# Kernel tuning notes

Measured on AMD Instinct MI355X. Metric: run time of the kernel, lower is better.

## Reference

```python
import jax, jax.numpy as jnp
import numpy as np

OMEGA = 1.5

def _sine(x, W, b, omega=OMEGA):
    return jnp.sin(omega * (x @ W.T + b))

def setup_inputs() -> dict:
    key = jax.random.key(0)
    ks = jax.random.split(key, 17)
    I = J = K = 384
    mid, R = 256, 100
    s = 0.05  # small init scale, mimics uniform(-1/in, 1/in) style init
    return {
        "A_input": jax.random.normal(ks[0], (I, 1), jnp.float32),
        "B_input": jax.random.normal(ks[1], (J, 1), jnp.float32),
        "C_input": jax.random.normal(ks[2], (K, 1), jnp.float32),
        "A_W1": jax.random.normal(ks[3], (mid, 1), jnp.float32) * s,
        "A_b1": jax.random.normal(ks[4], (mid,), jnp.float32) * s,
        "A_W2": jax.random.normal(ks[5], (R, mid), jnp.float32) * s,
        "A_b2": jax.random.normal(ks[6], (R,), jnp.float32) * s,
        "B_W1": jax.random.normal(ks[7], (mid, 1), jnp.float32) * s,
        "B_b1": jax.random.normal(ks[8], (mid,), jnp.float32) * s,
        "B_W2": jax.random.normal(ks[9], (R, mid), jnp.float32) * s,
        "B_b2": jax.random.normal(ks[10], (R,), jnp.float32) * s,
        "C_W1": jax.random.normal(ks[11], (mid, 1), jnp.float32) * s,
        "C_b1": jax.random.normal(ks[12], (mid,), jnp.float32) * s,
        "C_W2": jax.random.normal(ks[13], (mid, mid), jnp.float32) * s,
        "C_b2": jax.random.normal(ks[14], (mid,), jnp.float32) * s,
        "C_W3": jax.random.normal(ks[15], (R, mid), jnp.float32) * s,
        "C_b3": jax.random.normal(ks[16], (R,), jnp.float32) * s,
    }

def reference(A_input, B_input, C_input,
              A_W1, A_b1, A_W2, A_b2,
              B_W1, B_b1, B_W2, B_b2,
              C_W1, C_b1, C_W2, C_b2, C_W3, C_b3):
    # Factor networks
    A = _sine(A_input, A_W1, A_b1) @ A_W2.T + A_b2                  # [I, R]
    B = _sine(B_input, B_W1, B_b1) @ B_W2.T + B_b2                  # [J, R]
    C = _sine(_sine(C_input, C_W1, C_b1), C_W2, C_b2) @ C_W3.T + C_b3  # [K, R]
    # The frozen core is super-diagonal (core[r,r,r]=1), so the permute/matmul
    # chain reduces exactly to the CP contraction sum_r A[i,r]*B[j,r]*C[k,r].
    return jnp.einsum('ir,jr,kr->ijk', A, B, C)  # [I, J, K]
```

## Files before the change

kernel.cpp:

```cpp
#include <hip/hip_runtime.h>
#include <hip/hip_bf16.h>

#define RR 100
#define MID 256
#define NN 384
#define KP 128

typedef __attribute__((ext_vector_type(8))) __bf16 bf16x8;
typedef __attribute__((ext_vector_type(4))) float floatx4;
typedef unsigned short ushort_t;

#define SW(row, ch) ((((row) << 7)) + ((((ch) ^ ((row) & 15))) << 3))

__device__ __forceinline__ ushort_t f2bf(float f) {
  __hip_bfloat16 h = __float2bfloat16(f);
  return __builtin_bit_cast(ushort_t, h);
}

__global__ __launch_bounds__(256) void factors_kernel(
    const float* __restrict__ xA, const float* __restrict__ xB,
    const float* __restrict__ xC,
    const float* __restrict__ AW1, const float* __restrict__ Ab1,
    const float* __restrict__ AW2, const float* __restrict__ Ab2,
    const float* __restrict__ BW1, const float* __restrict__ Bb1,
    const float* __restrict__ BW2, const float* __restrict__ Bb2,
    const float* __restrict__ CW1, const float* __restrict__ Cb1,
    const float* __restrict__ CW2, const float* __restrict__ Cb2,
    const float* __restrict__ CW3, const float* __restrict__ Cb3,
    float* __restrict__ Af, float* __restrict__ Bf,
    ushort_t* __restrict__ Cbf) {
  __shared__ float h[MID];
  __shared__ float h2[MID];
  const int i = blockIdx.x;
  const int net = blockIdx.y;
  const int t = threadIdx.x;

  const float* x  = (net == 0) ? xA  : (net == 1) ? xB  : xC;
  const float* W1 = (net == 0) ? AW1 : (net == 1) ? BW1 : CW1;
  const float* b1 = (net == 0) ? Ab1 : (net == 1) ? Bb1 : Cb1;

  const float xv = x[i];
  h[t] = sinf(1.5f * (xv * W1[t] + b1[t]));
  __syncthreads();

  const float* hlast = h;
  if (net == 2) {
    float acc = Cb2[t];
    const float* __restrict__ w = &CW2[t * MID];
#pragma unroll 4
    for (int m = 0; m < MID; m += 4) {
      const float4 wv = *(const float4*)&w[m];
      const float4 hv = *(const float4*)&h[m];
      acc += hv.x * wv.x;
      acc += hv.y * wv.y;
      acc += hv.z * wv.z;
      acc += hv.w * wv.w;
    }
    h2[t] = sinf(1.5f * acc);
    __syncthreads();
    hlast = h2;
  }

  const float* W2 = (net == 0) ? AW2 : (net == 1) ? BW2 : CW3;
  const float* b2 = (net == 0) ? Ab2 : (net == 1) ? Bb2 : Cb3;

  if (t < KP) {
    float v = 0.0f;
    if (t < RR) {
      float acc = b2[t];
      const float* __restrict__ w = &W2[t * MID];
#pragma unroll 4
      for (int m = 0; m < MID; m += 4) {
        const float4 wv = *(const float4*)&w[m];
        const float4 hv = *(const float4*)&hlast[m];
        acc += hv.x * wv.x;
        acc += hv.y * wv.y;
        acc += hv.z * wv.z;
        acc += hv.w * wv.w;
      }
      v = acc;
    }
    if (net == 0)      Af[i * KP + t] = v;
    else if (net == 1) Bf[i * KP + t] = v;
    else               Cbf[i * KP + t] = f2bf(v);
  }
}

__global__ __launch_bounds__(256, 3) void cp_mfma(
    const float* __restrict__ Af, const float* __restrict__ Bf,
    const ushort_t* __restrict__ Cbf, float* __restrict__ out) {
  __shared__ ushort_t Wt[64 * KP];
  __shared__ ushort_t Ct[128 * KP];

  const int bid = blockIdx.x;
  const int swz = (bid & 7) * 288 + (bid >> 3);
  const int i   = swz / 6;
  const int j0  = (swz % 6) * 64;
  const int t   = threadIdx.x;

  {
    const int jx = t >> 2;
    const int q  = t & 3;
    const float* __restrict__ arow = Af + (size_t)i * KP + q * 32;
    const float* __restrict__ brow = Bf + (size_t)(j0 + jx) * KP + q * 32;
#pragma unroll
    for (int c = 0; c < 4; ++c) {
      const float4 a0 = *(const float4*)(arow + c * 8);
      const float4 a1 = *(const float4*)(arow + c * 8 + 4);
      const float4 b0 = *(const float4*)(brow + c * 8);
      const float4 b1 = *(const float4*)(brow + c * 8 + 4);
      uint4 wv;
      wv.x = (unsigned)f2bf(a0.x * b0.x) | ((unsigned)f2bf(a0.y * b0.y) << 16);
      wv.y = (unsigned)f2bf(a0.z * b0.z) | ((unsigned)f2bf(a0.w * b0.w) << 16);
      wv.z = (unsigned)f2bf(a1.x * b1.x) | ((unsigned)f2bf(a1.y * b1.y) << 16);
      wv.w = (unsigned)f2bf(a1.z * b1.z) | ((unsigned)f2bf(a1.w * b1.w) << 16);
      *(uint4*)&Wt[SW(jx, q * 4 + c)] = wv;
    }
  }

  const int lane = t & 63;
  const int w    = t >> 6;
  const int m16  = lane & 15;
  const int g    = lane >> 4;
  const int jrow = j0 + w * 16 + m16;
  const size_t obase = (size_t)i * NN * NN + (size_t)jrow * NN;

#pragma unroll 1
  for (int kt = 0; kt < 3; ++kt) {
    __syncthreads();

#pragma unroll
    for (int it = 0; it < 8; ++it) {
      const int idx = t + 256 * it;
      const int row = idx >> 4;
      const int ch  = idx & 15;
      *(uint4*)&Ct[SW(row, ch)] =
          *(const uint4*)&Cbf[(size_t)(kt * 128 + row) * KP + ch * 8];
    }
    __syncthreads();

    floatx4 acc[8];
#pragma unroll
    for (int kf = 0; kf < 8; ++kf) acc[kf] = (floatx4)0.0f;

#pragma unroll
    for (int ks = 0; ks < 4; ++ks) {
      const bf16x8 wfr = *(const bf16x8*)&Wt[SW(w * 16 + m16, ks * 4 + g)];
#pragma unroll
      for (int kf = 0; kf < 8; ++kf) {
        const bf16x8 cf = *(const bf16x8*)&Ct[SW(kf * 16 + m16, ks * 4 + g)];
        acc[kf] = __builtin_amdgcn_mfma_f32_16x16x32_bf16(
            cf, wfr, acc[kf], 0, 0, 0);
      }
    }

    const int kb = kt * 128 + g * 4;
#pragma unroll
    for (int kf = 0; kf < 8; ++kf) {
      *(floatx4*)&out[obase + kb + kf * 16] = acc[kf];
    }
  }
}

extern "C" void kernel_launch(void* const* d_in, const int* in_sizes, int n_in,
                              void* d_out, int out_size, void* d_ws, size_t ws_size,
                              hipStream_t stream) {
  const float* A_input = (const float*)d_in[0];
  const float* B_input = (const float*)d_in[1];
  const float* C_input = (const float*)d_in[2];
  const float* A_W1 = (const float*)d_in[3];
  const float* A_b1 = (const float*)d_in[4];
  const float* A_W2 = (const float*)d_in[5];
  const float* A_b2 = (const float*)d_in[6];
  const float* B_W1 = (const float*)d_in[7];
  const float* B_b1 = (const float*)d_in[8];
  const float* B_W2 = (const float*)d_in[9];
  const float* B_b2 = (const float*)d_in[10];
  const float* C_W1 = (const float*)d_in[11];
  const float* C_b1 = (const float*)d_in[12];
  const float* C_W2 = (const float*)d_in[13];
  const float* C_b2 = (const float*)d_in[14];
  const float* C_W3 = (const float*)d_in[15];
  const float* C_b3 = (const float*)d_in[16];

  float* Af = (float*)d_ws;
  float* Bf = Af + NN * KP;
  ushort_t* Cbf = (ushort_t*)(Bf + NN * KP);

  dim3 fgrid(NN, 3);
  factors_kernel<<<fgrid, 256, 0, stream>>>(
      A_input, B_input, C_input,
      A_W1, A_b1, A_W2, A_b2,
      B_W1, B_b1, B_W2, B_b2,
      C_W1, C_b1, C_W2, C_b2, C_W3, C_b3,
      Af, Bf, Cbf);

  cp_mfma<<<dim3((NN / 64) * NN), 256, 0, stream>>>(Af, Bf, Cbf, (float*)d_out);
}
```

Baseline: 292.8 us.

## Register-prefetch next C tile while computing current tile in cp_mfma

Unrolls the three k-tiles of the CP contraction and double-buffers the C tile through registers. The next tile's global loads are issued before the current tile's MFMA and store phase, hiding global latency. It also hoists the W fragments into registers once and reorders the MFMA loop so each output fragment is finished and stored right away, which lowers accumulator register pressure. The cost is extra VGPRs for the two uint4[8] buffers, which may hurt occupancy, and the kernel is output-store bound, so the benefit may be small.

New measurement: 345.6 us. 1.18x slower.

```diff
diff --git a/kernel.cpp b/kernel.cpp
--- a/kernel.cpp
+++ b/kernel.cpp
@@ -125,41 +125,69 @@
   const int jrow = j0 + w * 16 + m16;
   const size_t obase = (size_t)i * NN * NN + (size_t)jrow * NN;
 
-#pragma unroll 1
-  for (int kt = 0; kt < 3; ++kt) {
-    __syncthreads();
-
+  const int crow = t >> 4;
+  const int cch  = t & 15;
+  const ushort_t* __restrict__ csrc = Cbf + (size_t)crow * KP + cch * 8;
+  const int swbase = SW(crow, cch);
+
+  uint4 ca[8], cb[8];
 #pragma unroll
-    for (int it = 0; it < 8; ++it) {
-      const int idx = t + 256 * it;
-      const int row = idx >> 4;
-      const int ch  = idx & 15;
-      *(uint4*)&Ct[SW(row, ch)] =
-          *(const uint4*)&Cbf[(size_t)(kt * 128 + row) * KP + ch * 8];
-    }
-    __syncthreads();
-
-    floatx4 acc[8];
+  for (int it = 0; it < 8; ++it)
+    ca[it] = *(const uint4*)(csrc + (size_t)(16 * it) * KP);
+
+#define DS_WRITE(BUF)                                                        \
+  {                                                                          \
+    _Pragma("unroll") for (int it = 0; it < 8; ++it) {                       \
+      *(uint4*)&Ct[SW(crow + 16 * it, cch)] = BUF[it];                       \
+    }                                                                        \
+  }
+
+#define PREFETCH(BUF, KT)                                                    \
+  {                                                                          \
+    _Pragma("unroll") for (int it = 0; it < 8; ++it) {                       \
+      BUF[it] = *(const uint4*)(csrc + (size_t)((KT) * 128 + 16 * it) * KP); \
+    }                                                                        \
+  }
+
+#define COMPUTE_STORE(KT)                                                    \
+  {                                                                          \
+    const int kb = (KT) * 128 + g * 4;                                       \
+    _Pragma("unroll") for (int kf = 0; kf < 8; ++kf) {                       \
+      floatx4 a = (floatx4)0.0f;                                             \
+      _Pragma("unroll") for (int ks = 0; ks < 4; ++ks) {                     \
+        const bf16x8 cf =                                                    \
+            *(const bf16x8*)&Ct[SW(kf * 16 + m16, ks * 4 + g)];              \
+        a = __builtin_amdgcn_mfma_f32_16x16x32_bf16(cf, wfr[ks], a, 0, 0, 0);\
+      }                                                                      \
+      *(floatx4*)&out[obase + kb + kf * 16] = a;                             \
+    }                                                                        \
+  }
+
+  DS_WRITE(ca);
+  PREFETCH(cb, 1);
+  __syncthreads();
+
+  bf16x8 wfr[4];
 #pragma unroll
-    for (int kf = 0; kf < 8; ++kf) acc[kf] = (floatx4)0.0f;
-
-#pragma unroll
-    for (int ks = 0; ks < 4; ++ks) {
-      const bf16x8 wfr = *(const bf16x8*)&Wt[SW(w * 16 + m16, ks * 4 + g)];
-#pragma unroll
-      for (int kf = 0; kf < 8; ++kf) {
-        const bf16x8 cf = *(const bf16x8*)&Ct[SW(kf * 16 + m16, ks * 4 + g)];
-        acc[kf] = __builtin_amdgcn_mfma_f32_16x16x32_bf16(
-            cf, wfr, acc[kf], 0, 0, 0);
-      }
-    }
-
-    const int kb = kt * 128 + g * 4;
-#pragma unroll
-    for (int kf = 0; kf < 8; ++kf) {
-      *(floatx4*)&out[obase + kb + kf * 16] = acc[kf];
-    }
-  }
+  for (int ks = 0; ks < 4; ++ks)
+    wfr[ks] = *(const bf16x8*)&Wt[SW(w * 16 + m16, ks * 4 + g)];
+
+  COMPUTE_STORE(0);
+
+  __syncthreads();
+  DS_WRITE(cb);
+  PREFETCH(ca, 2);
+  __syncthreads();
+  COMPUTE_STORE(1);
+
+  __syncthreads();
+  DS_WRITE(ca);
+  __syncthreads();
+  COMPUTE_STORE(2);
+
+#undef DS_WRITE
+#undef PREFETCH
+#undef COMPUTE_STORE
 }
 
 extern "C" void kernel_launch(void* const* d_in, const int* in_sizes, int n_in,
```

## Stage output tile through LDS for coalesced stores and reorganize MFMA register blocking

Applied to the files above, without the earlier changes.

Instead of each lane writing scattered 16-byte fragments straight from MFMA accumulators, the kernel now writes results into the reused C tile in shared memory with an XOR swizzle. It then reads them back so each row of 128 floats goes to global memory as contiguous 512-byte segments. W fragments are hoisted into registers once, and each wave now computes a 4x2 tile (all j rows, 32 k columns) rather than 1x8. The next C tile is loaded between the readback and the global stores. This adds extra LDS traffic and barriers per k-tile in exchange for better-coalesced output writes on this write-bound kernel.

Result: no change. 290.5 us (-0.8%).

```diff
diff --git a/kernel.cpp b/kernel.cpp
--- a/kernel.cpp
+++ b/kernel.cpp
@@ -89,8 +89,9 @@
 __global__ __launch_bounds__(256, 3) void cp_mfma(
     const float* __restrict__ Af, const float* __restrict__ Bf,
     const ushort_t* __restrict__ Cbf, float* __restrict__ out) {
-  __shared__ ushort_t Wt[64 * KP];
-  __shared__ ushort_t Ct[128 * KP];
+  __shared__ __align__(16) ushort_t Wt[64 * KP];
+  __shared__ __align__(16) ushort_t Ct[128 * KP];
+  float* Ot = reinterpret_cast<float*>(Ct);
 
   const int bid = blockIdx.x;
   const int swz = (bid & 7) * 288 + (bid >> 3);
@@ -122,43 +123,84 @@
   const int w    = t >> 6;
   const int m16  = lane & 15;
   const int g    = lane >> 4;
-  const int jrow = j0 + w * 16 + m16;
-  const size_t obase = (size_t)i * NN * NN + (size_t)jrow * NN;
+
+  const int crow = t >> 4;
+  const int cch  = t & 15;
+  const ushort_t* __restrict__ csrc = Cbf + (size_t)crow * KP + cch * 8;
+
+  const int orow = t >> 5;
+  const int och  = t & 31;
+  const size_t obase0 = (size_t)i * NN * NN + (size_t)j0 * NN;
+
+#define STAGE(KT)                                                            \
+  {                                                                          \
+    _Pragma("unroll") for (int it = 0; it < 8; ++it) {                       \
+      *(uint4*)&Ct[SW(crow + 16 * it, cch)] =                                \
+          *(const uint4*)(csrc + (size_t)((KT) * 128 + 16 * it) * KP);       \
+    }                                                                        \
+  }
+
+  STAGE(0);
+  __syncthreads();
+
+  bf16x8 wfr[4][4];
+#pragma unroll
+  for (int jf = 0; jf < 4; ++jf)
+#pragma unroll
+    for (int ks = 0; ks < 4; ++ks)
+      wfr[jf][ks] = *(const bf16x8*)&Wt[SW(jf * 16 + m16, ks * 4 + g)];
 
 #pragma unroll 1
   for (int kt = 0; kt < 3; ++kt) {
-    __syncthreads();
-
+    floatx4 acc[4][2];
+#pragma unroll
+    for (int jf = 0; jf < 4; ++jf)
+#pragma unroll
+      for (int kf = 0; kf < 2; ++kf) acc[jf][kf] = (floatx4)0.0f;
+
+#pragma unroll
+    for (int ks = 0; ks < 4; ++ks) {
+      bf16x8 cf[2];
+#pragma unroll
+      for (int kf = 0; kf < 2; ++kf)
+        cf[kf] = *(const bf16x8*)&Ct[SW(w * 32 + kf * 16 + m16, ks * 4 + g)];
+#pragma unroll
+      for (int jf = 0; jf < 4; ++jf)
+#pragma unroll
+        for (int kf = 0; kf < 2; ++kf)
+          acc[jf][kf] = __builtin_amdgcn_mfma_f32_16x16x32_bf16(
+              cf[kf], wfr[jf][ks], acc[jf][kf], 0, 0, 0);
+    }
+    __syncthreads();
+
+#pragma unroll
+    for (int jf = 0; jf < 4; ++jf) {
+      const int row = jf * 16 + m16;
+#pragma unroll
+      for (int kf = 0; kf < 2; ++kf) {
+        const int ch = (w * 8 + kf * 4 + g) ^ (row & 7);
+        *(floatx4*)&Ot[row * 128 + ch * 4] = acc[jf][kf];
+      }
+    }
+    __syncthreads();
+
+    floatx4 o[8];
 #pragma unroll
     for (int it = 0; it < 8; ++it) {
-      const int idx = t + 256 * it;
-      const int row = idx >> 4;
-      const int ch  = idx & 15;
-      *(uint4*)&Ct[SW(row, ch)] =
-          *(const uint4*)&Cbf[(size_t)(kt * 128 + row) * KP + ch * 8];
-    }
-    __syncthreads();
-
-    floatx4 acc[8];
-#pragma unroll
-    for (int kf = 0; kf < 8; ++kf) acc[kf] = (floatx4)0.0f;
-
-#pragma unroll
-    for (int ks = 0; ks < 4; ++ks) {
-      const bf16x8 wfr = *(const bf16x8*)&Wt[SW(w * 16 + m16, ks * 4 + g)];
-#pragma unroll
-      for (int kf = 0; kf < 8; ++kf) {
-        const bf16x8 cf = *(const bf16x8*)&Ct[SW(kf * 16 + m16, ks * 4 + g)];
-        acc[kf] = __builtin_amdgcn_mfma_f32_16x16x32_bf16(
-            cf, wfr, acc[kf], 0, 0, 0);
-      }
-    }
-
-    const int kb = kt * 128 + g * 4;
-#pragma unroll
-    for (int kf = 0; kf < 8; ++kf) {
-      *(floatx4*)&out[obase + kb + kf * 16] = acc[kf];
-    }
+      const int r = orow + 8 * it;
+      const int c = och ^ (r & 7);
+      o[it] = *(const floatx4*)&Ot[r * 128 + c * 4];
+    }
+    __syncthreads();
+
+    if (kt == 0) { STAGE(1); }
+    else if (kt == 1) { STAGE(2); }
+#pragma unroll
+    for (int it = 0; it < 8; ++it) {
+      const int r = orow + 8 * it;
+      *(floatx4*)&out[obase0 + (size_t)r * NN + kt * 128 + och * 4] = o[it];
+    }
+    if (kt < 2) __syncthreads();
   }
 }
 
```
